# Performance work log

Measured on AMD Instinct MI355X. Metric: run time of the kernel, lower is better.

Reference implementation:

```python
import jax, jax.numpy as jnp
import numpy as np

N_NODES = 100000

def _sage(x, src, tgt, Wl, bl, Wr):
    # PyG SAGEConv (mean aggr): out = lin_l(mean_{j in N(i)} x_j) + lin_r(x_i)
    msg = x[src]                                             # [E, F] gather
    s = jax.ops.segment_sum(msg, tgt, num_segments=N_NODES)  # [N, F]
    cnt = jax.ops.segment_sum(jnp.ones((src.shape[0], 1), x.dtype), tgt, num_segments=N_NODES)
    agg = s / jnp.maximum(cnt, 1.0)
    return agg @ Wl + bl + x @ Wr


def setup_inputs() -> dict:
    key = jax.random.key(0)
    ks = jax.random.split(key, 16)
    node_dim, edge_dim, hidden = 128, 16, 64
    E = 1000000
    x = jax.random.normal(ks[0], (N_NODES, node_dim), jnp.float32)
    edge_index = jax.random.randint(ks[1], (2, E), 0, N_NODES, jnp.int64)
    edge_attr = jax.random.normal(ks[2], (E, edge_dim), jnp.float32)
    def lin(k, fi, fo, scale=None):
        s = scale if scale is not None else 1.0 / np.sqrt(fi)
        return jax.random.uniform(k, (fi, fo), jnp.float32, -s, s)
    return {
        "x": x, "edge_index": edge_index, "edge_attr": edge_attr,
        # edge MLP: Linear(16,64) -> ReLU -> Linear(64,64)
        "We1": lin(ks[3], edge_dim, hidden), "be1": jnp.zeros((hidden,), jnp.float32),
        "We2": lin(ks[4], hidden, hidden),   "be2": jnp.zeros((hidden,), jnp.float32),
        # SAGEConv 0: lin_l (with bias, on aggregated) + lin_r (no bias, on root)
        "Wl0": lin(ks[5], node_dim, hidden), "bl0": jnp.zeros((hidden,), jnp.float32),
        "Wr0": lin(ks[6], node_dim, hidden),
        # SAGEConv 1
        "Wl1": lin(ks[7], hidden, hidden), "bl1": jnp.zeros((hidden,), jnp.float32),
        "Wr1": lin(ks[8], hidden, hidden),
        # output MLP: Linear(64,64) -> ReLU -> (Dropout eval=id) -> Linear(64,1)
        "Wo1": lin(ks[9], hidden, hidden), "bo1": jnp.zeros((hidden,), jnp.float32),
        "Wo2": lin(ks[10], hidden, 1),     "bo2": jnp.zeros((1,), jnp.float32),
    }


def reference(x, edge_index, edge_attr, We1, be1, We2, be2,
              Wl0, bl0, Wr0, Wl1, bl1, Wr1, Wo1, bo1, Wo2, bo2):
    src, tgt = edge_index[0], edge_index[1]
    # edge MLP (dropout in eval mode = identity)
    ea = jax.nn.relu(edge_attr @ We1 + be1) @ We2 + be2       # [E, H]
    # two SAGE layers with ReLU
    h = jax.nn.relu(_sage(x, src, tgt, Wl0, bl0, Wr0))        # [N, H]
    h = jax.nn.relu(_sage(h, src, tgt, Wl1, bl1, Wr1))        # [N, H]
    # per-edge features: gather both endpoints + edge embedding
    ef = h[src] + h[tgt] + ea                                 # [E, H]
    out = jax.nn.relu(ef @ Wo1 + bo1) @ Wo2 + bo2             # [E, 1]
    return jax.nn.sigmoid(out[:, 0])                          # [E]
```

## Files before the change

kernel.cpp:

```cpp
#include <hip/hip_runtime.h>
#include <math.h>

typedef __attribute__((ext_vector_type(8))) short short8;
typedef __attribute__((ext_vector_type(4))) float f32x4;

#define CAPB 4096
#define CAPPB 48
#define NDECP 256

static __device__ __forceinline__ unsigned short f2bf(float f) {
  union { float f; unsigned int u; } x; x.f = f;
  unsigned int r = x.u + 0x7fffu + ((x.u >> 16) & 1u);
  return (unsigned short)(r >> 16);
}
static __device__ __forceinline__ float bf2f(unsigned int u) {
  union { unsigned int u; float f; } x; x.u = u << 16; return x.f;
}

__global__ void k_flag(const unsigned int* __restrict__ w, int nSample,
                       unsigned int* __restrict__ flag) {
  __shared__ unsigned int red[256];
  unsigned int v = 0;
  for (int i = threadIdx.x; i < nSample; i += 256) v |= w[2 * i + 1];
  red[threadIdx.x] = v;
  __syncthreads();
  for (int s = 128; s > 0; s >>= 1) {
    if (threadIdx.x < s) red[threadIdx.x] |= red[threadIdx.x + s];
    __syncthreads();
  }
  if (threadIdx.x == 0) flag[0] = red[0];
}

template <int K, bool BF16IN, int NTILES, bool INLINEW>
__device__ __forceinline__ void ngemm_body(
    const void* __restrict__ Xv, const unsigned short* __restrict__ WnT,
    const float* __restrict__ W0f, const float* __restrict__ W1f,
    unsigned short* __restrict__ Y0, unsigned short* __restrict__ Y1,
    int N, int blk, unsigned short* __restrict__ sX) {
  constexpr int STR = K + 8;
  constexpr int NC = K / 32;
  const int tid = threadIdx.x;
  const int wv = tid >> 6, lane = tid & 63;
  const int m = lane & 15, q = lane >> 4;
  const int row0 = blk * 64;

  short8 bB[NTILES][NC];
#pragma unroll
  for (int ct = 0; ct < NTILES; ++ct)
#pragma unroll
    for (int c = 0; c < NC; ++c) {
      if constexpr (INLINEW) {
        int n = (NTILES == 2) ? (wv * 32 + ct * 16 + m) : (wv * 16 + m);
        const float* Wf = (n < 64) ? W0f : W1f;
        int nn = n & 63;
        union { short8 s; unsigned short h[8]; } ub;
#pragma unroll
        for (int j = 0; j < 8; ++j)
          ub.h[j] = f2bf(Wf[(size_t)(c * 32 + q * 8 + j) * 64 + nn]);
        bB[ct][c] = ub.s;
      } else {
        int n = (NTILES == 2) ? (wv * 32 + ct * 16 + m) : (wv * 16 + m);
        bB[ct][c] = *(const short8*)(WnT + (size_t)n * K + c * 32 + q * 8);
      }
    }

#pragma unroll
  for (int i = 0; i < K / 16; ++i) {
    int f = tid + 256 * i;
    int r = f / (K / 4);
    int c4 = f % (K / 4);
    int rr = row0 + r; if (rr >= N) rr = N - 1;
    uint2 pk;
    if constexpr (BF16IN) {
      pk = *(const uint2*)((const unsigned short*)Xv + (size_t)rr * K + c4 * 4);
    } else {
      float4 v = *(const float4*)((const float*)Xv + (size_t)rr * K + c4 * 4);
      pk.x = (unsigned int)f2bf(v.x) | ((unsigned int)f2bf(v.y) << 16);
      pk.y = (unsigned int)f2bf(v.z) | ((unsigned int)f2bf(v.w) << 16);
    }
    *(uint2*)(sX + r * STR + c4 * 4) = pk;
  }
  __syncthreads();

  f32x4 acc[4][NTILES];
#pragma unroll
  for (int rt = 0; rt < 4; ++rt)
#pragma unroll
    for (int ct = 0; ct < NTILES; ++ct)
#pragma unroll
      for (int r = 0; r < 4; ++r) acc[rt][ct][r] = 0.f;

#pragma unroll
  for (int c = 0; c < NC; ++c) {
    short8 a[4];
#pragma unroll
    for (int rt = 0; rt < 4; ++rt)
      a[rt] = *(const short8*)(sX + (rt * 16 + m) * STR + c * 32 + q * 8);
#pragma unroll
    for (int rt = 0; rt < 4; ++rt)
#pragma unroll
      for (int ct = 0; ct < NTILES; ++ct)
        acc[rt][ct] = __builtin_amdgcn_mfma_f32_16x16x32_bf16(a[rt], bB[ct][c], acc[rt][ct], 0, 0, 0);
  }

#pragma unroll
  for (int rt = 0; rt < 4; ++rt)
#pragma unroll
    for (int ct = 0; ct < NTILES; ++ct) {
      unsigned short* Yw;
      int n;
      if constexpr (NTILES == 2) {
        Yw = (wv < 2) ? Y0 : Y1;
        n = (wv & 1) * 32 + ct * 16 + m;
      } else {
        Yw = Y0;
        n = wv * 16 + m;
      }
#pragma unroll
      for (int reg = 0; reg < 4; ++reg) {
        int row = row0 + rt * 16 + q * 4 + reg;
        if (row < N) Yw[(size_t)row * 64 + n] = f2bf(acc[rt][ct][reg]);
      }
    }
}

template <int K, bool BF16IN, int NTILES>
__global__ __launch_bounds__(256) void k_ngemm(
    const void* __restrict__ Xv, const unsigned short* __restrict__ WnT,
    unsigned short* __restrict__ Y0, unsigned short* __restrict__ Y1, int N) {
  __shared__ __align__(16) unsigned short sX[64 * (K + 8)];
  ngemm_body<K, BF16IN, NTILES, false>(Xv, WnT, nullptr, nullptr, Y0, Y1, N,
                                       blockIdx.x, sX);
}

__global__ __launch_bounds__(256) void k_mega1(
    const unsigned int* __restrict__ w, const unsigned int* __restrict__ flag,
    int E, int nDec, int nWork, int gB, int nConvThreads,
    int* __restrict__ src, int* __restrict__ tgt,
    int* __restrict__ counts, unsigned int* __restrict__ tmp,
    const float* __restrict__ x, unsigned short* __restrict__ Yl,
    unsigned short* __restrict__ Yr, int N,
    const float* __restrict__ We2, const float* __restrict__ Wo1,
    const float* __restrict__ be2, const float* __restrict__ bo1,
    const float* __restrict__ We1,
    const float* __restrict__ Wl0, const float* __restrict__ Wr0,
    const float* __restrict__ Wl1, const float* __restrict__ Wr1,
    unsigned short* __restrict__ W25T, unsigned short* __restrict__ We1T,
    unsigned short* __restrict__ Wo1T, float* __restrict__ cvec,
    unsigned short* __restrict__ WnT1,
    const float4* __restrict__ ef, uint2* __restrict__ eb) {
  __shared__ __align__(16) char smem[64 * 136 * 2];
  const int tid = threadIdx.x;
  const int tot = nDec + nWork;
  const int di  = (int)(((long long)blockIdx.x * nDec) / tot);
  const int di1 = (int)(((long long)(blockIdx.x + 1) * nDec) / tot);

  if (di1 > di) {
    int* hist = (int*)smem;
    hist[tid] = 0; hist[tid + 256] = 0;
    __syncthreads();
    const int e0 = di * 4096;
    const int e1 = (e0 + 4096 < E) ? (e0 + 4096) : E;
    const unsigned int fl = flag[0];
    for (int e = e0 + tid; e < e1; e += 256) {
      int s, t;
      if (fl) { s = (int)w[e]; t = (int)w[E + e]; }
      else    { s = (int)w[2 * e]; t = (int)w[2 * (E + e)]; }
      src[e] = s; tgt[e] = t;
      atomicAdd(hist + (t >> 8), 1);
    }
    __syncthreads();
    {
      int c0 = hist[tid], c1 = hist[tid + 256];
      counts[(size_t)tid * NDECP + di] = c0;
      counts[(size_t)(tid + 256) * NDECP + di] = c1;
      __syncthreads();
      hist[tid] = 0; hist[tid + 256] = 0;
    }
    __syncthreads();
    for (int e = e0 + tid; e < e1; e += 256) {
      int s, t;
      if (fl) { s = (int)w[e]; t = (int)w[E + e]; }
      else    { s = (int)w[2 * e]; t = (int)w[2 * (E + e)]; }
      int b = t >> 8;
      int pos = atomicAdd(hist + b, 1);
      if (pos < CAPPB)
        tmp[((size_t)b * NDECP + di) * CAPPB + pos] =
            ((unsigned int)s << 8) | (unsigned int)(t & 255);
    }
    return;
  }
  const int wi = blockIdx.x - di;
  if (wi == 0) {
    float* sB = (float*)smem;
    for (int i = tid; i < 1024; i += 256)
      *(float4*)&sB[i * 4] = *(const float4*)(Wo1 + i * 4);
    __syncthreads();
    for (int idx = tid; idx < 4096; idx += 256) {
      int k = idx >> 6, n = idx & 63;
      float s = 0.f;
#pragma unroll 8
      for (int mm = 0; mm < 64; ++mm) s = fmaf(We2[k * 64 + mm], sB[mm * 64 + n], s);
      W25T[n * 64 + k] = f2bf(s);
      Wo1T[n * 64 + k] = f2bf(sB[k * 64 + n]);
    }
    for (int idx = tid; idx < 2048; idx += 256) {
      int n = idx >> 5, k = idx & 31;
      We1T[n * 32 + k] = (k < 16) ? f2bf(We1[k * 64 + n]) : (unsigned short)0;
    }
    if (tid < 64) {
      float s = bo1[tid];
#pragma unroll 8
      for (int mm = 0; mm < 64; ++mm) s = fmaf(be2[mm], sB[mm * 64 + tid], s);
      cvec[tid] = s;
    }
  } else if (wi <= 32) {
    int idx = (wi - 1) * 256 + tid;
    int n = idx >> 6, k = idx & 63;
    float v = (n < 64) ? Wl1[(size_t)k * 64 + n] : Wr1[(size_t)k * 64 + (n - 64)];
    WnT1[idx] = f2bf(v);
  } else if (wi < 33 + gB) {
    ngemm_body<128, false, 2, true>(x, nullptr, Wl0, Wr0, Yl, Yr, N,
                                    wi - 33, (unsigned short*)smem);
  } else {
    int gid = (wi - 33 - gB) * 256 + tid;
    int nItems = E * 4;
    for (int i = gid; i < nItems; i += nConvThreads) {
      float4 v = ef[i];
      uint2 pk;
      pk.x = (unsigned int)f2bf(v.x) | ((unsigned int)f2bf(v.y) << 16);
      pk.y = (unsigned int)f2bf(v.z) | ((unsigned int)f2bf(v.w) << 16);
      eb[i] = pk;
    }
  }
}

__global__ __launch_bounds__(256) void k_bsort(
    const unsigned int* __restrict__ tmp, const int* __restrict__ counts,
    int* __restrict__ csrc, uint2* __restrict__ rowptr2, int N, int nDec) {
  __shared__ int cnt[256];
  __shared__ int curs[256];
  __shared__ int wsum[4];
  __shared__ int scnt[NDECP];
  const int b = blockIdx.x, tid = threadIdx.x;
  scnt[tid] = (tid < nDec) ? counts[(size_t)b * NDECP + tid] : 0;
  cnt[tid] = 0;
  __syncthreads();
  const unsigned int* reg = tmp + (size_t)b * NDECP * CAPPB;
  const int nSlots = nDec * CAPPB;
  for (int idx = tid; idx < nSlots; idx += 256) {
    int blk = idx / CAPPB, j = idx - blk * CAPPB;
    if (j < scnt[blk]) atomicAdd(&cnt[reg[idx] & 255u], 1);
  }
  __syncthreads();
  const int lane = tid & 63, wv = tid >> 6;
  int v = cnt[tid];
  int incl = v;
#pragma unroll
  for (int off = 1; off < 64; off <<= 1) {
    int t = __shfl_up(incl, off, 64);
    if (lane >= off) incl += t;
  }
  if (lane == 63) wsum[wv] = incl;
  __syncthreads();
  int add = 0;
  for (int ww = 0; ww < wv; ++ww) add += wsum[ww];
  int excl = add + incl - v;
  curs[tid] = excl;
  int node = b * 256 + tid;
  if (node < N)
    rowptr2[node] = make_uint2((unsigned int)(b * CAPB + excl),
                               (unsigned int)(b * CAPB + excl + v));
  __syncthreads();
  for (int idx = tid; idx < nSlots; idx += 256) {
    int blk = idx / CAPPB, j = idx - blk * CAPPB;
    if (j < scnt[blk]) {
      unsigned int wd = reg[idx];
      int p = atomicAdd(&curs[wd & 255u], 1);
      csrc[(size_t)b * CAPB + p] = (int)(wd >> 8);
    }
  }
}

__global__ __launch_bounds__(256) void k_agg(
    const unsigned short* __restrict__ Y, const uint2* __restrict__ rowptr2,
    const int* __restrict__ csrc, const float* __restrict__ bias,
    const unsigned short* __restrict__ Yr, unsigned short* __restrict__ H,
    int N) {
  int node = (blockIdx.x * 256 + threadIdx.x) >> 6;
  if (node >= N) return;
  const int lane = threadIdx.x & 63;
  const int c4 = lane & 15, rr = lane >> 4;
  uint2 be = rowptr2[node];
  int beg = (int)be.x, end = (int)be.y;
  float a0 = 0.f, a1 = 0.f, a2 = 0.f, a3 = 0.f;
  float b0 = 0.f, b1 = 0.f, b2 = 0.f, b3 = 0.f;
  for (int e = beg; e < end; e += 8) {
    int e0 = e + rr, e1 = e + 4 + rr;
    if (e0 < end) {
      int s = csrc[e0];
      uint2 v = *(const uint2*)(Y + (size_t)s * 64 + c4 * 4);
      a0 += bf2f(v.x & 0xffffu); a1 += bf2f(v.x >> 16);
      a2 += bf2f(v.y & 0xffffu); a3 += bf2f(v.y >> 16);
    }
    if (e1 < end) {
      int s = csrc[e1];
      uint2 v = *(const uint2*)(Y + (size_t)s * 64 + c4 * 4);
      b0 += bf2f(v.x & 0xffffu); b1 += bf2f(v.x >> 16);
      b2 += bf2f(v.y & 0xffffu); b3 += bf2f(v.y >> 16);
    }
  }
  a0 += b0; a1 += b1; a2 += b2; a3 += b3;
#pragma unroll
  for (int msk = 16; msk <= 32; msk <<= 1) {
    a0 += __shfl_xor(a0, msk, 64);
    a1 += __shfl_xor(a1, msk, 64);
    a2 += __shfl_xor(a2, msk, 64);
    a3 += __shfl_xor(a3, msk, 64);
  }
  if (rr == 0) {
    float cdeg = (float)(end - beg);
    if (cdeg < 1.f) cdeg = 1.f;
    float inv = 1.f / cdeg;
    float4 bv = *(const float4*)(bias + c4 * 4);
    uint2 yv = *(const uint2*)(Yr + (size_t)node * 64 + c4 * 4);
    float o0 = fmaxf(a0 * inv + bv.x + bf2f(yv.x & 0xffffu), 0.f);
    float o1 = fmaxf(a1 * inv + bv.y + bf2f(yv.x >> 16), 0.f);
    float o2 = fmaxf(a2 * inv + bv.z + bf2f(yv.y & 0xffffu), 0.f);
    float o3 = fmaxf(a3 * inv + bv.w + bf2f(yv.y >> 16), 0.f);
    uint2 pk;
    pk.x = (unsigned int)f2bf(o0) | ((unsigned int)f2bf(o1) << 16);
    pk.y = (unsigned int)f2bf(o2) | ((unsigned int)f2bf(o3) << 16);
    *(uint2*)(H + (size_t)node * 64 + c4 * 4) = pk;
  }
}

#define T1_STRIDE 72
#define G_STRIDE 68
__global__ __launch_bounds__(256) void k_edge3(
    const unsigned short* __restrict__ EAb, const int* __restrict__ src,
    const int* __restrict__ tgt, const unsigned short* __restrict__ Gb,
    const unsigned short* __restrict__ We1T,
    const unsigned short* __restrict__ W25T,
    const float* __restrict__ cvec, const float* __restrict__ be1,
    const float* __restrict__ Wo2, const float* __restrict__ bo2,
    float* __restrict__ out, int E, int nT, int nWaves) {
  __shared__ unsigned short sT1a[4][16 * T1_STRIDE];
  __shared__ float sGa[4][16 * G_STRIDE];
  const int tid = threadIdx.x;
  const int wid = tid >> 6, lane = tid & 63;
  const int m = lane & 15, q = lane >> 4;
  unsigned short* sT1 = sT1a[wid];
  float* sG = sGa[wid];

  short8 bWe1[4], bW25[4][2];
  float cv[4], wo2v[4], be1v[4];
#pragma unroll
  for (int nt = 0; nt < 4; ++nt) {
    int n = nt * 16 + m;
    bWe1[nt] = *(const short8*)(We1T + n * 32 + q * 8);
    bW25[nt][0] = *(const short8*)(W25T + n * 64 + q * 8);
    bW25[nt][1] = *(const short8*)(W25T + n * 64 + 32 + q * 8);
    cv[nt] = cvec[n];
    wo2v[nt] = Wo2[n];
    be1v[nt] = be1[n];
  }
  const float b_out = bo2[0];
  const short8 zfrag = {};

  int t = blockIdx.x * 4 + wid;
  if (t >= nT) return;
  int il = t * 16 + m; if (il >= E) il = E - 1;
  int my_idx = (lane < 16) ? src[il] : ((lane < 32) ? tgt[il] : 0);

  while (true) {
    const int base = t * 16;
    const int tn = t + nWaves;
    const bool last = (tn >= nT);
    const int tc = last ? t : tn;

    int il_n = tc * 16 + m; if (il_n >= E) il_n = E - 1;
    int idx_n = (lane < 16) ? src[il_n] : ((lane < 32) ? tgt[il_n] : 0);

    int rs[4], rt[4];
#pragma unroll
    for (int r = 0; r < 4; ++r) {
      rs[r] = __shfl(my_idx, q * 4 + r, 64);
      rt[r] = __shfl(my_idx, 16 + q * 4 + r, 64);
    }
    uint2 sv[4], tv[4];
#pragma unroll
    for (int r = 0; r < 4; ++r) {
      sv[r] = *(const uint2*)(Gb + (size_t)rs[r] * 64 + m * 4);
      tv[r] = *(const uint2*)(Gb + (size_t)rt[r] * 64 + m * 4);
    }

    int er = base + m; if (er >= E) er = E - 1;
    short8 aEA = zfrag;
    if (q < 2) aEA = *(const short8*)(EAb + (size_t)er * 16 + (q & 1) * 8);

    f32x4 t1[4];
#pragma unroll
    for (int nt = 0; nt < 4; ++nt) {
      f32x4 cinit; cinit[0] = be1v[nt]; cinit[1] = be1v[nt];
      cinit[2] = be1v[nt]; cinit[3] = be1v[nt];
      t1[nt] = __builtin_amdgcn_mfma_f32_16x16x32_bf16(aEA, bWe1[nt], cinit, 0, 0, 0);
    }
#pragma unroll
    for (int nt = 0; nt < 4; ++nt)
#pragma unroll
      for (int r = 0; r < 4; ++r)
        sT1[(q * 4 + r) * T1_STRIDE + nt * 16 + m] = f2bf(fmaxf(t1[nt][r], 0.f));
    short8 aT0 = *(short8*)(sT1 + m * T1_STRIDE + q * 8);
    short8 aT1 = *(short8*)(sT1 + m * T1_STRIDE + 32 + q * 8);

#pragma unroll
    for (int r = 0; r < 4; ++r) {
      f32x4 g;
      g[0] = bf2f(sv[r].x & 0xffffu) + bf2f(tv[r].x & 0xffffu);
      g[1] = bf2f(sv[r].x >> 16)     + bf2f(tv[r].x >> 16);
      g[2] = bf2f(sv[r].y & 0xffffu) + bf2f(tv[r].y & 0xffffu);
      g[3] = bf2f(sv[r].y >> 16)     + bf2f(tv[r].y >> 16);
      *(f32x4*)(sG + (q * 4 + r) * G_STRIDE + m * 4) = g;
    }

    f32x4 acc[4];
#pragma unroll
    for (int nt = 0; nt < 4; ++nt)
#pragma unroll
      for (int r = 0; r < 4; ++r)
        acc[nt][r] = cv[nt] + sG[(q * 4 + r) * G_STRIDE + nt * 16 + m];
#pragma unroll
    for (int nt = 0; nt < 4; ++nt) {
      acc[nt] = __builtin_amdgcn_mfma_f32_16x16x32_bf16(aT0, bW25[nt][0], acc[nt], 0, 0, 0);
      acc[nt] = __builtin_amdgcn_mfma_f32_16x16x32_bf16(aT1, bW25[nt][1], acc[nt], 0, 0, 0);
    }

    float p[4];
#pragma unroll
    for (int r = 0; r < 4; ++r) {
      p[r] = fmaxf(acc[0][r], 0.f) * wo2v[0] + fmaxf(acc[1][r], 0.f) * wo2v[1] +
             fmaxf(acc[2][r], 0.f) * wo2v[2] + fmaxf(acc[3][r], 0.f) * wo2v[3];
    }
#pragma unroll
    for (int msk = 1; msk <= 8; msk <<= 1) {
#pragma unroll
      for (int r = 0; r < 4; ++r) p[r] += __shfl_xor(p[r], msk, 64);
    }
    if (m == 0) {
#pragma unroll
      for (int r = 0; r < 4; ++r) {
        int row = base + q * 4 + r;
        if (row < E) out[row] = 1.f / (1.f + __expf(-(p[r] + b_out)));
      }
    }

    if (last) break;
    t = tn; my_idx = idx_n;
  }
}

extern "C" void kernel_launch(void* const* d_in, const int* in_sizes, int n_in,
                              void* d_out, int out_size, void* d_ws, size_t ws_size,
                              hipStream_t stream) {
  const float* x     = (const float*)d_in[0];
  const unsigned int* eidx = (const unsigned int*)d_in[1];
  const float* eattr = (const float*)d_in[2];
  const float* We1 = (const float*)d_in[3];
  const float* be1 = (const float*)d_in[4];
  const float* We2 = (const float*)d_in[5];
  const float* be2 = (const float*)d_in[6];
  const float* Wl0 = (const float*)d_in[7];
  const float* bl0 = (const float*)d_in[8];
  const float* Wr0 = (const float*)d_in[9];
  const float* Wl1 = (const float*)d_in[10];
  const float* bl1 = (const float*)d_in[11];
  const float* Wr1 = (const float*)d_in[12];
  const float* Wo1 = (const float*)d_in[13];
  const float* bo1 = (const float*)d_in[14];
  const float* Wo2 = (const float*)d_in[15];
  const float* bo2 = (const float*)d_in[16];

  const int N = in_sizes[0] / 128;
  const int E = in_sizes[2] / 16;
  const int NBUCK = (N + 255) >> 8;
  float* out = (float*)d_out;

  char* ws = (char*)d_ws;
  size_t off = 0;
  auto alloc = [&](size_t bytes) {
    char* p = ws + off;
    off += (bytes + 255) & ~(size_t)255;
    return p;
  };
  unsigned int* flag = (unsigned int*)alloc(256);
  int* src    = (int*)alloc((size_t)E * 4);
  int* tgt    = (int*)alloc((size_t)E * 4);
  int* counts = (int*)alloc((size_t)512 * NDECP * 4);
  unsigned int* tmp = (unsigned int*)alloc((size_t)NBUCK * NDECP * CAPPB * 4);
  int* csrc   = (int*)alloc((size_t)NBUCK * CAPB * 4);
  uint2* rowptr2 = (uint2*)alloc((size_t)N * 8);
  unsigned short* EAb = (unsigned short*)alloc((size_t)E * 16 * 2);
  unsigned short* Hb = (unsigned short*)alloc((size_t)N * 64 * 2);
  unsigned short* Yl = (unsigned short*)alloc((size_t)N * 64 * 2);
  unsigned short* Yr = (unsigned short*)alloc((size_t)N * 64 * 2);
  unsigned short* Gb = (unsigned short*)alloc((size_t)N * 64 * 2);
  unsigned short* W25T = (unsigned short*)alloc(64 * 64 * 2);
  unsigned short* We1T = (unsigned short*)alloc(64 * 32 * 2);
  unsigned short* Wo1T = (unsigned short*)alloc(64 * 64 * 2);
  unsigned short* WnT1 = (unsigned short*)alloc(128 * 64 * 2);
  float* cvec = (float*)alloc(64 * 4);
  (void)ws_size; (void)n_in; (void)out_size;

  k_flag<<<1, 256, 0, stream>>>(eidx, 8192, flag);

  const int nDec = (E + 4095) / 4096;
  const int gB = (N + 63) / 64;
  const int convB = 1024;
  const int nWork = 33 + gB + convB;
  k_mega1<<<nDec + nWork, 256, 0, stream>>>(
      eidx, flag, E, nDec, nWork, gB, convB * 256,
      src, tgt, counts, tmp,
      x, Yl, Yr, N,
      We2, Wo1, be2, bo1, We1, Wl0, Wr0, Wl1, Wr1,
      W25T, We1T, Wo1T, cvec, WnT1,
      (const float4*)eattr, (uint2*)EAb);

  k_bsort<<<NBUCK, 256, 0, stream>>>(tmp, counts, csrc, rowptr2, N, nDec);

  const int aggB = (N + 3) / 4;
  k_agg<<<aggB, 256, 0, stream>>>(Yl, rowptr2, csrc, bl0, Yr, Hb, N);

  k_ngemm<64, true, 2><<<gB, 256, 0, stream>>>(Hb, WnT1, Yl, Yr, N);
  k_agg<<<aggB, 256, 0, stream>>>(Yl, rowptr2, csrc, bl1, Yr, Hb, N);

  k_ngemm<64, true, 1><<<gB, 256, 0, stream>>>(Hb, Wo1T, Gb, nullptr, N);

  const int nT = (E + 15) / 16;
  const int blocks = 3072;
  k_edge3<<<blocks, 256, 0, stream>>>(EAb, src, tgt, Gb, We1T, W25T, cvec,
                                      be1, Wo2, bo2, out, E, nT, blocks * 4);
}
```

Measured before the change: 429.6 us.

## Split fused mega kernel into separate decode, convert, prep and GEMM launches

Breaks the heterogeneous k_mega1 kernel into four sequential launches: edge-index decode/bucketing, edge-attr bf16 conversion, weight preparation (now also pretransposing layer-0 weights into WnT0), and a standalone layer-0 node GEMM. The GEMM no longer converts fp32 weights inline per block. The aim is to drop the per-block branch dispatch and inline weight conversion, and to give each phase a uniform kernel. In exchange it adds launch overhead and loses the overlap of independent work that the fused kernel gave within one grid.

```diff
diff --git a/kernel.cpp b/kernel.cpp
--- a/kernel.cpp
+++ b/kernel.cpp
@@ -31,37 +31,125 @@
   if (threadIdx.x == 0) flag[0] = red[0];
 }
 
-template <int K, bool BF16IN, int NTILES, bool INLINEW>
-__device__ __forceinline__ void ngemm_body(
+__global__ __launch_bounds__(256) void k_decode(
+    const unsigned int* __restrict__ w, const unsigned int* __restrict__ flag,
+    int E, int* __restrict__ src, int* __restrict__ tgt,
+    int* __restrict__ counts, unsigned int* __restrict__ tmp) {
+  __shared__ int hist[512];
+  const int tid = threadIdx.x;
+  const int di = blockIdx.x;
+  hist[tid] = 0; hist[tid + 256] = 0;
+  __syncthreads();
+  const int e0 = di * 4096;
+  const int e1 = (e0 + 4096 < E) ? (e0 + 4096) : E;
+  const unsigned int fl = flag[0];
+  for (int e = e0 + tid; e < e1; e += 256) {
+    int s, t;
+    if (fl) { s = (int)w[e]; t = (int)w[E + e]; }
+    else    { s = (int)w[2 * e]; t = (int)w[2 * (E + e)]; }
+    src[e] = s; tgt[e] = t;
+    atomicAdd(hist + (t >> 8), 1);
+  }
+  __syncthreads();
+  {
+    int c0 = hist[tid], c1 = hist[tid + 256];
+    counts[(size_t)tid * NDECP + di] = c0;
+    counts[(size_t)(tid + 256) * NDECP + di] = c1;
+    __syncthreads();
+    hist[tid] = 0; hist[tid + 256] = 0;
+  }
+  __syncthreads();
+  for (int e = e0 + tid; e < e1; e += 256) {
+    int s, t;
+    if (fl) { s = (int)w[e]; t = (int)w[E + e]; }
+    else    { s = (int)w[2 * e]; t = (int)w[2 * (E + e)]; }
+    int b = t >> 8;
+    int pos = atomicAdd(hist + b, 1);
+    if (pos < CAPPB)
+      tmp[((size_t)b * NDECP + di) * CAPPB + pos] =
+          ((unsigned int)s << 8) | (unsigned int)(t & 255);
+  }
+}
+
+__global__ __launch_bounds__(256) void k_conv(
+    const float4* __restrict__ ef, uint2* __restrict__ eb, int nItems,
+    int nThreads) {
+  int gid = blockIdx.x * 256 + threadIdx.x;
+  for (int i = gid; i < nItems; i += nThreads) {
+    float4 v = ef[i];
+    uint2 pk;
+    pk.x = (unsigned int)f2bf(v.x) | ((unsigned int)f2bf(v.y) << 16);
+    pk.y = (unsigned int)f2bf(v.z) | ((unsigned int)f2bf(v.w) << 16);
+    eb[i] = pk;
+  }
+}
+
+__global__ __launch_bounds__(256) void k_prep(
+    const float* __restrict__ We2, const float* __restrict__ Wo1,
+    const float* __restrict__ be2, const float* __restrict__ bo1,
+    const float* __restrict__ We1,
+    const float* __restrict__ Wl0, const float* __restrict__ Wr0,
+    const float* __restrict__ Wl1, const float* __restrict__ Wr1,
+    unsigned short* __restrict__ W25T, unsigned short* __restrict__ We1T,
+    unsigned short* __restrict__ Wo1T, float* __restrict__ cvec,
+    unsigned short* __restrict__ WnT1, unsigned short* __restrict__ WnT0) {
+  const int tid = threadIdx.x;
+  const int b = blockIdx.x;
+  if (b == 0) {
+    __shared__ float sB[4096];
+    for (int i = tid; i < 1024; i += 256)
+      *(float4*)&sB[i * 4] = *(const float4*)(Wo1 + i * 4);
+    __syncthreads();
+    for (int idx = tid; idx < 4096; idx += 256) {
+      int k = idx >> 6, n = idx & 63;
+      float s = 0.f;
+#pragma unroll 8
+      for (int mm = 0; mm < 64; ++mm) s = fmaf(We2[k * 64 + mm], sB[mm * 64 + n], s);
+      W25T[n * 64 + k] = f2bf(s);
+      Wo1T[n * 64 + k] = f2bf(sB[k * 64 + n]);
+    }
+    for (int idx = tid; idx < 2048; idx += 256) {
+      int n = idx >> 5, k = idx & 31;
+      We1T[n * 32 + k] = (k < 16) ? f2bf(We1[k * 64 + n]) : (unsigned short)0;
+    }
+    if (tid < 64) {
+      float s = bo1[tid];
+#pragma unroll 8
+      for (int mm = 0; mm < 64; ++mm) s = fmaf(be2[mm], sB[mm * 64 + tid], s);
+      cvec[tid] = s;
+    }
+  } else if (b <= 32) {
+    int idx = (b - 1) * 256 + tid;
+    int n = idx >> 6, k = idx & 63;
+    float v = (n < 64) ? Wl1[(size_t)k * 64 + n] : Wr1[(size_t)k * 64 + (n - 64)];
+    WnT1[idx] = f2bf(v);
+  } else {
+    int idx = (b - 33) * 256 + tid;
+    int n = idx >> 7, k = idx & 127;
+    float v = (n < 64) ? Wl0[(size_t)k * 64 + n] : Wr0[(size_t)k * 64 + (n - 64)];
+    WnT0[idx] = f2bf(v);
+  }
+}
+
+template <int K, bool BF16IN, int NTILES>
+__global__ __launch_bounds__(256) void k_ngemm(
     const void* __restrict__ Xv, const unsigned short* __restrict__ WnT,
-    const float* __restrict__ W0f, const float* __restrict__ W1f,
-    unsigned short* __restrict__ Y0, unsigned short* __restrict__ Y1,
-    int N, int blk, unsigned short* __restrict__ sX) {
+    unsigned short* __restrict__ Y0, unsigned short* __restrict__ Y1, int N) {
   constexpr int STR = K + 8;
   constexpr int NC = K / 32;
+  __shared__ __align__(16) unsigned short sX[64 * STR];
   const int tid = threadIdx.x;
   const int wv = tid >> 6, lane = tid & 63;
   const int m = lane & 15, q = lane >> 4;
-  const int row0 = blk * 64;
+  const int row0 = blockIdx.x * 64;
 
   short8 bB[NTILES][NC];
 #pragma unroll
   for (int ct = 0; ct < NTILES; ++ct)
 #pragma unroll
     for (int c = 0; c < NC; ++c) {
-      if constexpr (INLINEW) {
-        int n = (NTILES == 2) ? (wv * 32 + ct * 16 + m) : (wv * 16 + m);
-        const float* Wf = (n < 64) ? W0f : W1f;
-        int nn = n & 63;
-        union { short8 s; unsigned short h[8]; } ub;
-#pragma unroll
-        for (int j = 0; j < 8; ++j)
-          ub.h[j] = f2bf(Wf[(size_t)(c * 32 + q * 8 + j) * 64 + nn]);
-        bB[ct][c] = ub.s;
-      } else {
-        int n = (NTILES == 2) ? (wv * 32 + ct * 16 + m) : (wv * 16 + m);
-        bB[ct][c] = *(const short8*)(WnT + (size_t)n * K + c * 32 + q * 8);
-      }
+      int n = (NTILES == 2) ? (wv * 32 + ct * 16 + m) : (wv * 16 + m);
+      bB[ct][c] = *(const short8*)(WnT + (size_t)n * K + c * 32 + q * 8);
     }
 
 #pragma unroll
@@ -122,117 +210,6 @@
         if (row < N) Yw[(size_t)row * 64 + n] = f2bf(acc[rt][ct][reg]);
       }
     }
-}
-
-template <int K, bool BF16IN, int NTILES>
-__global__ __launch_bounds__(256) void k_ngemm(
-    const void* __restrict__ Xv, const unsigned short* __restrict__ WnT,
-    unsigned short* __restrict__ Y0, unsigned short* __restrict__ Y1, int N) {
-  __shared__ __align__(16) unsigned short sX[64 * (K + 8)];
-  ngemm_body<K, BF16IN, NTILES, false>(Xv, WnT, nullptr, nullptr, Y0, Y1, N,
-                                       blockIdx.x, sX);
-}
-
-__global__ __launch_bounds__(256) void k_mega1(
-    const unsigned int* __restrict__ w, const unsigned int* __restrict__ flag,
-    int E, int nDec, int nWork, int gB, int nConvThreads,
-    int* __restrict__ src, int* __restrict__ tgt,
-    int* __restrict__ counts, unsigned int* __restrict__ tmp,
-    const float* __restrict__ x, unsigned short* __restrict__ Yl,
-    unsigned short* __restrict__ Yr, int N,
-    const float* __restrict__ We2, const float* __restrict__ Wo1,
-    const float* __restrict__ be2, const float* __restrict__ bo1,
-    const float* __restrict__ We1,
-    const float* __restrict__ Wl0, const float* __restrict__ Wr0,
-    const float* __restrict__ Wl1, const float* __restrict__ Wr1,
-    unsigned short* __restrict__ W25T, unsigned short* __restrict__ We1T,
-    unsigned short* __restrict__ Wo1T, float* __restrict__ cvec,
-    unsigned short* __restrict__ WnT1,
-    const float4* __restrict__ ef, uint2* __restrict__ eb) {
-  __shared__ __align__(16) char smem[64 * 136 * 2];
-  const int tid = threadIdx.x;
-  const int tot = nDec + nWork;
-  const int di  = (int)(((long long)blockIdx.x * nDec) / tot);
-  const int di1 = (int)(((long long)(blockIdx.x + 1) * nDec) / tot);
-
-  if (di1 > di) {
-    int* hist = (int*)smem;
-    hist[tid] = 0; hist[tid + 256] = 0;
-    __syncthreads();
-    const int e0 = di * 4096;
-    const int e1 = (e0 + 4096 < E) ? (e0 + 4096) : E;
-    const unsigned int fl = flag[0];
-    for (int e = e0 + tid; e < e1; e += 256) {
-      int s, t;
-      if (fl) { s = (int)w[e]; t = (int)w[E + e]; }
-      else    { s = (int)w[2 * e]; t = (int)w[2 * (E + e)]; }
-      src[e] = s; tgt[e] = t;
-      atomicAdd(hist + (t >> 8), 1);
-    }
-    __syncthreads();
-    {
-      int c0 = hist[tid], c1 = hist[tid + 256];
-      counts[(size_t)tid * NDECP + di] = c0;
-      counts[(size_t)(tid + 256) * NDECP + di] = c1;
-      __syncthreads();
-      hist[tid] = 0; hist[tid + 256] = 0;
-    }
-    __syncthreads();
-    for (int e = e0 + tid; e < e1; e += 256) {
-      int s, t;
-      if (fl) { s = (int)w[e]; t = (int)w[E + e]; }
-      else    { s = (int)w[2 * e]; t = (int)w[2 * (E + e)]; }
-      int b = t >> 8;
-      int pos = atomicAdd(hist + b, 1);
-      if (pos < CAPPB)
-        tmp[((size_t)b * NDECP + di) * CAPPB + pos] =
-            ((unsigned int)s << 8) | (unsigned int)(t & 255);
-    }
-    return;
-  }
-  const int wi = blockIdx.x - di;
-  if (wi == 0) {
-    float* sB = (float*)smem;
-    for (int i = tid; i < 1024; i += 256)
-      *(float4*)&sB[i * 4] = *(const float4*)(Wo1 + i * 4);
-    __syncthreads();
-    for (int idx = tid; idx < 4096; idx += 256) {
-      int k = idx >> 6, n = idx & 63;
-      float s = 0.f;
-#pragma unroll 8
-      for (int mm = 0; mm < 64; ++mm) s = fmaf(We2[k * 64 + mm], sB[mm * 64 + n], s);
-      W25T[n * 64 + k] = f2bf(s);
-      Wo1T[n * 64 + k] = f2bf(sB[k * 64 + n]);
-    }
-    for (int idx = tid; idx < 2048; idx += 256) {
-      int n = idx >> 5, k = idx & 31;
-      We1T[n * 32 + k] = (k < 16) ? f2bf(We1[k * 64 + n]) : (unsigned short)0;
-    }
-    if (tid < 64) {
-      float s = bo1[tid];
-#pragma unroll 8
-      for (int mm = 0; mm < 64; ++mm) s = fmaf(be2[mm], sB[mm * 64 + tid], s);
-      cvec[tid] = s;
-    }
-  } else if (wi <= 32) {
-    int idx = (wi - 1) * 256 + tid;
-    int n = idx >> 6, k = idx & 63;
-    float v = (n < 64) ? Wl1[(size_t)k * 64 + n] : Wr1[(size_t)k * 64 + (n - 64)];
-    WnT1[idx] = f2bf(v);
-  } else if (wi < 33 + gB) {
-    ngemm_body<128, false, 2, true>(x, nullptr, Wl0, Wr0, Yl, Yr, N,
-                                    wi - 33, (unsigned short*)smem);
-  } else {
-    int gid = (wi - 33 - gB) * 256 + tid;
-    int nItems = E * 4;
-    for (int i = gid; i < nItems; i += nConvThreads) {
-      float4 v = ef[i];
-      uint2 pk;
-      pk.x = (unsigned int)f2bf(v.x) | ((unsigned int)f2bf(v.y) << 16);
-      pk.y = (unsigned int)f2bf(v.z) | ((unsigned int)f2bf(v.w) << 16);
-      eb[i] = pk;
-    }
-  }
 }
 
 __global__ __launch_bounds__(256) void k_bsort(
@@ -509,22 +486,22 @@
   unsigned short* We1T = (unsigned short*)alloc(64 * 32 * 2);
   unsigned short* Wo1T = (unsigned short*)alloc(64 * 64 * 2);
   unsigned short* WnT1 = (unsigned short*)alloc(128 * 64 * 2);
+  unsigned short* WnT0 = (unsigned short*)alloc(128 * 128 * 2);
   float* cvec = (float*)alloc(64 * 4);
   (void)ws_size; (void)n_in; (void)out_size;
-
-  k_flag<<<1, 256, 0, stream>>>(eidx, 8192, flag);
 
   const int nDec = (E + 4095) / 4096;
   const int gB = (N + 63) / 64;
   const int convB = 1024;
-  const int nWork = 33 + gB + convB;
-  k_mega1<<<nDec + nWork, 256, 0, stream>>>(
-      eidx, flag, E, nDec, nWork, gB, convB * 256,
-      src, tgt, counts, tmp,
-      x, Yl, Yr, N,
-      We2, Wo1, be2, bo1, We1, Wl0, Wr0, Wl1, Wr1,
-      W25T, We1T, Wo1T, cvec, WnT1,
-      (const float4*)eattr, (uint2*)EAb);
+
+  k_flag<<<1, 256, 0, stream>>>(eidx, 8192, flag);
+
+  k_decode<<<nDec, 256, 0, stream>>>(eidx, flag, E, src, tgt, counts, tmp);
+  k_conv<<<convB, 256, 0, stream>>>((const float4*)eattr, (uint2*)EAb,
+                                    E * 4, convB * 256);
+  k_prep<<<97, 256, 0, stream>>>(We2, Wo1, be2, bo1, We1, Wl0, Wr0, Wl1, Wr1,
+                                 W25T, We1T, Wo1T, cvec, WnT1, WnT0);
+  k_ngemm<128, false, 2><<<gB, 256, 0, stream>>>(x, WnT0, Yl, Yr, N);
 
   k_bsort<<<NBUCK, 256, 0, stream>>>(tmp, counts, csrc, rowptr2, N, nDec);
 
```

Result: slower. 455.1 us (+5.9%).
